# Kernel optimization log

Measured on AMD Instinct MI355X. Metric: run time of the kernel, lower is better.

Reference implementation:

```python
import jax, jax.numpy as jnp
import numpy as np

T = 4096          # time steps
I = 3             # input_size
R = 4096          # reservoir_size
LEAK = 0.1        # leaking_rate
RHO = 0.9         # spectral_radius
SPARSITY = 0.5


def setup_inputs() -> dict:
    key = jax.random.key(0)
    k1, k2, k3, k4 = jax.random.split(key, 4)
    x = jax.random.normal(k1, (T, I), dtype=jnp.float32)
    Win = jax.random.uniform(k2, (R, I), minval=-0.5, maxval=0.5, dtype=jnp.float32)
    Wh = jax.random.uniform(k3, (R, R), minval=-0.5, maxval=0.5, dtype=jnp.float32)
    mask = (jax.random.uniform(k4, (R, R)) < SPARSITY).astype(jnp.float32)
    Wh_np = np.asarray(Wh * mask, dtype=np.float64)
    # rescale to spectral radius RHO (power iteration estimate of dominant |eig|)
    v = np.random.default_rng(0).normal(size=R)
    rho = 1.0
    for _ in range(100):
        v = Wh_np @ v
        rho = np.linalg.norm(v)
        v = v / rho
    Wh = jnp.asarray(Wh_np * (RHO / rho), dtype=jnp.float32)
    return {"x": x, "Win": Win, "Wh": Wh}


def reference(x, Win, Wh):
    # Precompute all input projections in one GEMM: [T, R]
    ux = x @ Win.T

    def step(h, u):
        h_new = jnp.tanh(u + Wh @ h)
        h = LEAK * h + (1.0 - LEAK) * h_new
        return h, h

    h0 = jnp.zeros((Wh.shape[0],), dtype=x.dtype)
    _, hs = jax.lax.scan(step, h0, ux)   # hs: [T, R]
    return jnp.concatenate([hs, x], axis=1)  # H: [T, R + I]
```

## Files before the change

### kernel.cpp

```cpp
#include <hip/hip_runtime.h>
#include <cmath>


#define T_STEPS  4096
#define R_SIZE   4096
#define I_SIZE   3
#define OUT_COLS (R_SIZE + I_SIZE)
#define NB       256
#define BT       256
#define RPB      16
#define RPW      4
#define NREP     16
#define LEAK     0.1f

typedef _Float16 h2 __attribute__((ext_vector_type(2)));
typedef _Float16 h8 __attribute__((ext_vector_type(8)));
typedef unsigned u32x2 __attribute__((ext_vector_type(2)));
typedef unsigned u32x4 __attribute__((ext_vector_type(4)));

__device__ __forceinline__ float fdot2f(h2 a, h2 b, float c) {
#if __has_builtin(__builtin_amdgcn_fdot2)
    return __builtin_amdgcn_fdot2(a, b, c, false);
#else
    return c + (float)a[0] * (float)b[0] + (float)a[1] * (float)b[1];
#endif
}

__device__ __forceinline__ float fast_tanhf(float s) {
    float av = __builtin_fabsf(s);
    float e  = __builtin_amdgcn_exp2f(-2.8853900817779268f * av);
    float r  = (1.0f - e) * __builtin_amdgcn_rcpf(1.0f + e);
    return __builtin_copysignf(r, s);
}

__device__ __forceinline__ void poll16(const unsigned* p0, const unsigned* p1,
                                       const unsigned* p2, const unsigned* p3,
                                       u32x4& a0, u32x4& a1, u32x4& a2, u32x4& a3) {
    asm volatile(
        "global_load_dwordx4 %0, %4, off sc0 sc1\n\t"
        "global_load_dwordx4 %1, %5, off sc0 sc1\n\t"
        "global_load_dwordx4 %2, %6, off sc0 sc1\n\t"
        "global_load_dwordx4 %3, %7, off sc0 sc1\n\t"
        "s_waitcnt vmcnt(0)"
        : "=&v"(a0), "=&v"(a1), "=&v"(a2), "=&v"(a3)
        : "v"(p0), "v"(p1), "v"(p2), "v"(p3)
        : "memory");
}

__device__ __forceinline__ unsigned tagbad4(const u32x4& a, unsigned tg2) {
    unsigned t01 = __builtin_amdgcn_perm(a[1], a[0], 0x07060302u) ^ tg2;
    unsigned t23 = __builtin_amdgcn_perm(a[3], a[2], 0x07060302u) ^ tg2;
    return t01 | t23;
}
__device__ __forceinline__ int check16(const u32x4& a0, const u32x4& a1,
                                       const u32x4& a2, const u32x4& a3,
                                       unsigned tg2) {
    unsigned bad = tagbad4(a0, tg2) | tagbad4(a1, tg2) |
                   tagbad4(a2, tg2) | tagbad4(a3, tg2);
    return bad == 0u;
}

template<int CTRL>
__device__ __forceinline__ float dpp_ror_add(float a) {
    int r = __builtin_amdgcn_update_dpp(0, __builtin_bit_cast(int, a),
                                        CTRL, 0xF, 0xF, false);
    return a + __builtin_bit_cast(float, r);
}
__device__ __forceinline__ float wave_sum(float a, int idx32, int idx48) {
    a = dpp_ror_add<0x128>(a);
    a = dpp_ror_add<0x124>(a);
    a = dpp_ror_add<0x122>(a);
    a = dpp_ror_add<0x121>(a);
    int ai = __builtin_bit_cast(int, a);
    float b = __builtin_bit_cast(float, __builtin_amdgcn_ds_swizzle(ai, 0x401F));
    float c = __builtin_bit_cast(float, __builtin_amdgcn_ds_bpermute(idx32, ai));
    float d = __builtin_bit_cast(float, __builtin_amdgcn_ds_bpermute(idx48, ai));
    return (a + b) + (c + d);
}

__global__ void __launch_bounds__(BT, 1) esn_kernel(
    const float* __restrict__ Wh,
    const float* __restrict__ Win,
    const float* __restrict__ x,
    float* __restrict__ out,
    unsigned* __restrict__ ex0,
    unsigned* __restrict__ ex1,
    unsigned rep_mask)
{
    __shared__ alignas(16) unsigned short hl[R_SIZE];
    __shared__ float xs[T_STEPS * I_SIZE];

    const int tid  = threadIdx.x;
    const int bid  = blockIdx.x;
    const int wv   = tid >> 6;
    const int lane = tid & 63;
    const int r0   = bid * RPB;
    const int idx32 = ((lane ^ 32) << 2);
    const int idx48 = ((lane ^ 48) << 2);

    h8 wreg[RPW * 8];
    #pragma unroll
    for (int rr = 0; rr < RPW; ++rr) {
        const float* src = Wh + (size_t)(r0 + wv * RPW + rr) * R_SIZE;
        #pragma unroll
        for (int j = 0; j < 8; ++j) {
            int e = (j * 64 + lane) * 8;
            float4 a = *(const float4*)(src + e);
            float4 b = *(const float4*)(src + e + 4);
            h8 hv;
            hv[0] = (_Float16)a.x; hv[1] = (_Float16)a.y;
            hv[2] = (_Float16)a.z; hv[3] = (_Float16)a.w;
            hv[4] = (_Float16)b.x; hv[5] = (_Float16)b.y;
            hv[6] = (_Float16)b.z; hv[7] = (_Float16)b.w;
            wreg[rr * 8 + j] = hv;
        }
    }

    for (int i = tid; i < T_STEPS * I_SIZE; i += BT) xs[i] = x[i];

    float win0 = 0.f, win1 = 0.f, win2 = 0.f;
    if (lane < RPW) {
        int r = r0 + wv * RPW + lane;
        win0 = Win[(size_t)r * I_SIZE + 0];
        win1 = Win[(size_t)r * I_SIZE + 1];
        win2 = Win[(size_t)r * I_SIZE + 2];
    }
    float hown = 0.0f;

    const unsigned rep  = (unsigned)bid & rep_mask;
    const unsigned nrep = rep_mask + 1u;
    const unsigned* pa[2][4];
    #pragma unroll
    for (int m = 0; m < 4; ++m) {
        pa[0][m] = ex0 + rep * R_SIZE + m * 1024 + tid * 4;
        pa[1][m] = ex1 + rep * R_SIZE + m * 1024 + tid * 4;
    }

    __syncthreads();

    unsigned long long tgt = 0;
    unsigned P = 0;

    for (int t = 0; t < T_STEPS; ++t) {
        const int par = t & 1;
        unsigned* __restrict__ exw = par ? ex0 : ex1;

        float u = 0.0f;
        if (lane < RPW)
            u = xs[t * 3 + 0] * win0 + xs[t * 3 + 1] * win1 +
                xs[t * 3 + 2] * win2;

        if (P) {
            for (int i = 0; i < 4096; ++i) {
                if (__builtin_amdgcn_s_memrealtime() >= tgt) break;
                __builtin_amdgcn_s_sleep(2);
            }
        }

        u32x4 a0, a1, a2, a3;
        const unsigned tg2 = (unsigned)t * 0x00010001u;
        poll16(pa[par][0], pa[par][1], pa[par][2], pa[par][3], a0, a1, a2, a3);
        int ok = check16(a0, a1, a2, a3, tg2);
        const int missed = !__all(ok);
        if (missed) {
            do {
                __builtin_amdgcn_s_sleep(1);
                if (!ok) {
                    poll16(pa[par][0], pa[par][1], pa[par][2], pa[par][3],
                           a0, a1, a2, a3);
                    ok = check16(a0, a1, a2, a3, tg2);
                }
            } while (!__all(ok));
        }

        {
            u32x4 aa[4] = {a0, a1, a2, a3};
            #pragma unroll
            for (int m = 0; m < 4; ++m) {
                u32x2 w;
                w[0] = __builtin_amdgcn_perm(aa[m][1], aa[m][0], 0x05040100u);
                w[1] = __builtin_amdgcn_perm(aa[m][3], aa[m][2], 0x05040100u);
                *(u32x2*)&hl[m * 1024 + tid * 4] = w;
            }
        }
        __syncthreads();

        h8 hreg[8];
        const h8* hl8 = (const h8*)hl;
        #pragma unroll
        for (int j = 0; j < 8; ++j) hreg[j] = hl8[j * 64 + lane];

        float acc[RPW];
        #pragma unroll
        for (int rr = 0; rr < RPW; ++rr) {
            float a = 0.0f;
            #pragma unroll
            for (int j = 0; j < 8; ++j) {
                h8 w8 = wreg[rr * 8 + j];
                h8 hh = hreg[j];
                a = fdot2f(__builtin_shufflevector(w8, w8, 0, 1),
                           __builtin_shufflevector(hh, hh, 0, 1), a);
                a = fdot2f(__builtin_shufflevector(w8, w8, 2, 3),
                           __builtin_shufflevector(hh, hh, 2, 3), a);
                a = fdot2f(__builtin_shufflevector(w8, w8, 4, 5),
                           __builtin_shufflevector(hh, hh, 4, 5), a);
                a = fdot2f(__builtin_shufflevector(w8, w8, 6, 7),
                           __builtin_shufflevector(hh, hh, 6, 7), a);
            }
            acc[rr] = wave_sum(a, idx32, idx48);
        }

        float hv = 0.0f;
        unsigned word = 0;
        if (lane < RPW) {
            float a = (lane == 0) ? acc[0]
                    : (lane == 1) ? acc[1]
                    : (lane == 2) ? acc[2] : acc[3];
            float hn = fast_tanhf(u + a);
            hv = LEAK * hown + (1.0f - LEAK) * hn;
            hown = hv;
            word = ((unsigned)(t + 1) << 16) |
                   (unsigned)__builtin_bit_cast(unsigned short, (_Float16)hv);
        }
        unsigned w0 = __shfl(word, 0, 64);
        unsigned w1 = __shfl(word, 1, 64);
        unsigned w2 = __shfl(word, 2, 64);
        unsigned w3 = __shfl(word, 3, 64);
        if ((unsigned)lane < nrep) {
            u32x4 pw = {w0, w1, w2, w3};
            unsigned* dst = exw + (unsigned)lane * R_SIZE + r0 + wv * RPW;
            asm volatile("global_store_dwordx4 %0, %1, off sc0 sc1"
                         :: "v"(dst), "v"(pw) : "memory");
        }

        {
            unsigned long long nowp = __builtin_amdgcn_s_memrealtime();
            P = missed ? (P + 8u > 2048u ? 2048u : P + 8u)
                       : (P >= 2u ? P - 2u : 0u);
            tgt = nowp + P;
        }

        if (lane < RPW) {
            out[(size_t)t * OUT_COLS + (r0 + wv * RPW + lane)] = hv;
        }
    }
}

__global__ void copy_x_kernel(const float* __restrict__ x, float* __restrict__ out) {
    int i = blockIdx.x * blockDim.x + threadIdx.x;
    if (i < T_STEPS * I_SIZE) {
        int t = i / I_SIZE, c = i % I_SIZE;
        out[(size_t)t * OUT_COLS + R_SIZE + c] = x[i];
    }
}

extern "C" void kernel_launch(void* const* d_in, const int* in_sizes, int n_in,
                              void* d_out, int out_size, void* d_ws, size_t ws_size,
                              hipStream_t stream) {
    const float* x   = (const float*)d_in[0];
    const float* Win = (const float*)d_in[1];
    const float* Wh  = (const float*)d_in[2];
    float* out = (float*)d_out;

    size_t need16 = (size_t)2 * 16 * R_SIZE * sizeof(unsigned);
    size_t need8  = (size_t)2 *  8 * R_SIZE * sizeof(unsigned);
    unsigned nrep = (ws_size >= need16) ? 16u : (ws_size >= need8 ? 8u : 1u);
    unsigned rep_mask = nrep - 1u;
    unsigned* ex0 = (unsigned*)d_ws;
    unsigned* ex1 = ex0 + (size_t)nrep * R_SIZE;

    (void)hipMemsetAsync(d_ws, 0, (size_t)2 * nrep * R_SIZE * sizeof(unsigned),
                         stream);

    copy_x_kernel<<<dim3((T_STEPS * I_SIZE + BT - 1) / BT), dim3(BT), 0, stream>>>(x, out);

    void* args[] = {(void*)&Wh, (void*)&Win, (void*)&x, (void*)&out,
                    (void*)&ex0, (void*)&ex1, (void*)&rep_mask};
    hipError_t e = hipLaunchCooperativeKernel((void*)esn_kernel, dim3(NB), dim3(BT),
                                              args, 0, stream);
    if (e != hipSuccess) {
        esn_kernel<<<dim3(NB), dim3(BT), 0, stream>>>(Wh, Win, x, out,
                                                      ex0, ex1, rep_mask);
    }
}
```

Baseline: 8.116 ms.

## Split dot-product across K within block, drop LDS staging of hidden state

Each thread now keeps 16 rows by 16 contiguous columns of Wh in registers and dots them directly with the polled hidden-state values. This removes the LDS staging of the full state vector and the barrier that followed it. Partial sums are reduced within 16-lane groups by DPP, then combined across the block through a small double-buffered LDS array after one barrier. Wave 0 alone computes tanh, publishes the tagged words and writes the output. The step's critical path now runs through that cross-wave reduction and a single-wave publish.

```diff
diff --git a/kernel.cpp b/kernel.cpp
--- a/kernel.cpp
+++ b/kernel.cpp
@@ -9,13 +9,10 @@
 #define NB       256
 #define BT       256
 #define RPB      16
-#define RPW      4
 #define NREP     16
 #define LEAK     0.1f
 
 typedef _Float16 h2 __attribute__((ext_vector_type(2)));
-typedef _Float16 h8 __attribute__((ext_vector_type(8)));
-typedef unsigned u32x2 __attribute__((ext_vector_type(2)));
 typedef unsigned u32x4 __attribute__((ext_vector_type(4)));
 
 __device__ __forceinline__ float fdot2f(h2 a, h2 b, float c) {
@@ -66,16 +63,16 @@
                                         CTRL, 0xF, 0xF, false);
     return a + __builtin_bit_cast(float, r);
 }
-__device__ __forceinline__ float wave_sum(float a, int idx32, int idx48) {
+__device__ __forceinline__ float group16_sum(float a) {
     a = dpp_ror_add<0x128>(a);
     a = dpp_ror_add<0x124>(a);
     a = dpp_ror_add<0x122>(a);
     a = dpp_ror_add<0x121>(a);
-    int ai = __builtin_bit_cast(int, a);
-    float b = __builtin_bit_cast(float, __builtin_amdgcn_ds_swizzle(ai, 0x401F));
-    float c = __builtin_bit_cast(float, __builtin_amdgcn_ds_bpermute(idx32, ai));
-    float d = __builtin_bit_cast(float, __builtin_amdgcn_ds_bpermute(idx48, ai));
-    return (a + b) + (c + d);
+    return a;
+}
+
+__device__ __forceinline__ h2 lo_pair(unsigned wa, unsigned wb) {
+    return __builtin_bit_cast(h2, __builtin_amdgcn_perm(wb, wa, 0x05040100u));
 }
 
 __global__ void __launch_bounds__(BT, 1) esn_kernel(
@@ -87,7 +84,7 @@
     unsigned* __restrict__ ex1,
     unsigned rep_mask)
 {
-    __shared__ alignas(16) unsigned short hl[R_SIZE];
+    __shared__ float comb[2][16][16];
     __shared__ float xs[T_STEPS * I_SIZE];
 
     const int tid  = threadIdx.x;
@@ -95,46 +92,40 @@
     const int wv   = tid >> 6;
     const int lane = tid & 63;
     const int r0   = bid * RPB;
-    const int idx32 = ((lane ^ 32) << 2);
-    const int idx48 = ((lane ^ 48) << 2);
-
-    h8 wreg[RPW * 8];
+
+    h2 wreg[RPB][8];
     #pragma unroll
-    for (int rr = 0; rr < RPW; ++rr) {
-        const float* src = Wh + (size_t)(r0 + wv * RPW + rr) * R_SIZE;
-        #pragma unroll
-        for (int j = 0; j < 8; ++j) {
-            int e = (j * 64 + lane) * 8;
-            float4 a = *(const float4*)(src + e);
-            float4 b = *(const float4*)(src + e + 4);
-            h8 hv;
-            hv[0] = (_Float16)a.x; hv[1] = (_Float16)a.y;
-            hv[2] = (_Float16)a.z; hv[3] = (_Float16)a.w;
-            hv[4] = (_Float16)b.x; hv[5] = (_Float16)b.y;
-            hv[6] = (_Float16)b.z; hv[7] = (_Float16)b.w;
-            wreg[rr * 8 + j] = hv;
-        }
+    for (int r = 0; r < RPB; ++r) {
+        const float* src = Wh + (size_t)(r0 + r) * R_SIZE + wv * 1024 + lane * 16;
+        float4 A = *(const float4*)(src + 0);
+        float4 B = *(const float4*)(src + 4);
+        float4 C = *(const float4*)(src + 8);
+        float4 D = *(const float4*)(src + 12);
+        wreg[r][0][0] = (_Float16)A.x; wreg[r][0][1] = (_Float16)A.y;
+        wreg[r][1][0] = (_Float16)A.z; wreg[r][1][1] = (_Float16)A.w;
+        wreg[r][2][0] = (_Float16)B.x; wreg[r][2][1] = (_Float16)B.y;
+        wreg[r][3][0] = (_Float16)B.z; wreg[r][3][1] = (_Float16)B.w;
+        wreg[r][4][0] = (_Float16)C.x; wreg[r][4][1] = (_Float16)C.y;
+        wreg[r][5][0] = (_Float16)C.z; wreg[r][5][1] = (_Float16)C.w;
+        wreg[r][6][0] = (_Float16)D.x; wreg[r][6][1] = (_Float16)D.y;
+        wreg[r][7][0] = (_Float16)D.z; wreg[r][7][1] = (_Float16)D.w;
     }
 
     for (int i = tid; i < T_STEPS * I_SIZE; i += BT) xs[i] = x[i];
 
     float win0 = 0.f, win1 = 0.f, win2 = 0.f;
-    if (lane < RPW) {
-        int r = r0 + wv * RPW + lane;
+    if (wv == 0 && lane < RPB) {
+        int r = r0 + lane;
         win0 = Win[(size_t)r * I_SIZE + 0];
         win1 = Win[(size_t)r * I_SIZE + 1];
         win2 = Win[(size_t)r * I_SIZE + 2];
     }
     float hown = 0.0f;
 
-    const unsigned rep  = (unsigned)bid & rep_mask;
-    const unsigned nrep = rep_mask + 1u;
-    const unsigned* pa[2][4];
-    #pragma unroll
-    for (int m = 0; m < 4; ++m) {
-        pa[0][m] = ex0 + rep * R_SIZE + m * 1024 + tid * 4;
-        pa[1][m] = ex1 + rep * R_SIZE + m * 1024 + tid * 4;
-    }
+    const unsigned rep = (unsigned)bid & rep_mask;
+    const unsigned* pb[2];
+    pb[0] = ex0 + rep * R_SIZE + wv * 1024 + lane * 16;
+    pb[1] = ex1 + rep * R_SIZE + wv * 1024 + lane * 16;
 
     __syncthreads();
 
@@ -146,7 +137,7 @@
         unsigned* __restrict__ exw = par ? ex0 : ex1;
 
         float u = 0.0f;
-        if (lane < RPW)
+        if (wv == 0 && lane < RPB)
             u = xs[t * 3 + 0] * win0 + xs[t * 3 + 1] * win1 +
                 xs[t * 3 + 2] * win2;
 
@@ -159,78 +150,71 @@
 
         u32x4 a0, a1, a2, a3;
         const unsigned tg2 = (unsigned)t * 0x00010001u;
-        poll16(pa[par][0], pa[par][1], pa[par][2], pa[par][3], a0, a1, a2, a3);
+        const unsigned* pp = pb[par];
+        poll16(pp, pp + 4, pp + 8, pp + 12, a0, a1, a2, a3);
         int ok = check16(a0, a1, a2, a3, tg2);
         const int missed = !__all(ok);
         if (missed) {
             do {
                 __builtin_amdgcn_s_sleep(1);
                 if (!ok) {
-                    poll16(pa[par][0], pa[par][1], pa[par][2], pa[par][3],
-                           a0, a1, a2, a3);
+                    poll16(pp, pp + 4, pp + 8, pp + 12, a0, a1, a2, a3);
                     ok = check16(a0, a1, a2, a3, tg2);
                 }
             } while (!__all(ok));
         }
 
-        {
-            u32x4 aa[4] = {a0, a1, a2, a3};
+        h2 hh[8];
+        hh[0] = lo_pair(a0[0], a0[1]); hh[1] = lo_pair(a0[2], a0[3]);
+        hh[2] = lo_pair(a1[0], a1[1]); hh[3] = lo_pair(a1[2], a1[3]);
+        hh[4] = lo_pair(a2[0], a2[1]); hh[5] = lo_pair(a2[2], a2[3]);
+        hh[6] = lo_pair(a3[0], a3[1]); hh[7] = lo_pair(a3[2], a3[3]);
+
+        float acc[RPB];
+        #pragma unroll
+        for (int r = 0; r < RPB; ++r) {
+            float s = 0.0f;
             #pragma unroll
-            for (int m = 0; m < 4; ++m) {
-                u32x2 w;
-                w[0] = __builtin_amdgcn_perm(aa[m][1], aa[m][0], 0x05040100u);
-                w[1] = __builtin_amdgcn_perm(aa[m][3], aa[m][2], 0x05040100u);
-                *(u32x2*)&hl[m * 1024 + tid * 4] = w;
+            for (int j = 0; j < 8; ++j)
+                s = fdot2f(wreg[r][j], hh[j], s);
+            acc[r] = group16_sum(s);
+        }
+
+        if ((lane & 15) == 0) {
+            const int c = wv * 4 + (lane >> 4);
+            float4* q = (float4*)&comb[par][c][0];
+            q[0] = make_float4(acc[0],  acc[1],  acc[2],  acc[3]);
+            q[1] = make_float4(acc[4],  acc[5],  acc[6],  acc[7]);
+            q[2] = make_float4(acc[8],  acc[9],  acc[10], acc[11]);
+            q[3] = make_float4(acc[12], acc[13], acc[14], acc[15]);
+        }
+        __syncthreads();
+
+        if (wv == 0) {
+            float hv = 0.0f;
+            unsigned word = 0;
+            if (lane < RPB) {
+                float s = 0.0f;
+                #pragma unroll
+                for (int c = 0; c < 16; ++c) s += comb[par][c][lane];
+                float hn = fast_tanhf(u + s);
+                hv = LEAK * hown + (1.0f - LEAK) * hn;
+                hown = hv;
+                word = ((unsigned)(t + 1) << 16) |
+                       (unsigned)__builtin_bit_cast(unsigned short, (_Float16)hv);
             }
-        }
-        __syncthreads();
-
-        h8 hreg[8];
-        const h8* hl8 = (const h8*)hl;
-        #pragma unroll
-        for (int j = 0; j < 8; ++j) hreg[j] = hl8[j * 64 + lane];
-
-        float acc[RPW];
-        #pragma unroll
-        for (int rr = 0; rr < RPW; ++rr) {
-            float a = 0.0f;
-            #pragma unroll
-            for (int j = 0; j < 8; ++j) {
-                h8 w8 = wreg[rr * 8 + j];
-                h8 hh = hreg[j];
-                a = fdot2f(__builtin_shufflevector(w8, w8, 0, 1),
-                           __builtin_shufflevector(hh, hh, 0, 1), a);
-                a = fdot2f(__builtin_shufflevector(w8, w8, 2, 3),
-                           __builtin_shufflevector(hh, hh, 2, 3), a);
-                a = fdot2f(__builtin_shufflevector(w8, w8, 4, 5),
-                           __builtin_shufflevector(hh, hh, 4, 5), a);
-                a = fdot2f(__builtin_shufflevector(w8, w8, 6, 7),
-                           __builtin_shufflevector(hh, hh, 6, 7), a);
+            const int rq = (lane & 3) * 4;
+            unsigned w0 = __shfl(word, rq + 0, 64);
+            unsigned w1 = __shfl(word, rq + 1, 64);
+            unsigned w2 = __shfl(word, rq + 2, 64);
+            unsigned w3 = __shfl(word, rq + 3, 64);
+            if ((unsigned)(lane >> 2) <= rep_mask) {
+                u32x4 pw = {w0, w1, w2, w3};
+                unsigned* dst = exw + (unsigned)(lane >> 2) * R_SIZE + r0 + rq;
+                asm volatile("global_store_dwordx4 %0, %1, off sc0 sc1"
+                             :: "v"(dst), "v"(pw) : "memory");
             }
-            acc[rr] = wave_sum(a, idx32, idx48);
-        }
-
-        float hv = 0.0f;
-        unsigned word = 0;
-        if (lane < RPW) {
-            float a = (lane == 0) ? acc[0]
-                    : (lane == 1) ? acc[1]
-                    : (lane == 2) ? acc[2] : acc[3];
-            float hn = fast_tanhf(u + a);
-            hv = LEAK * hown + (1.0f - LEAK) * hn;
-            hown = hv;
-            word = ((unsigned)(t + 1) << 16) |
-                   (unsigned)__builtin_bit_cast(unsigned short, (_Float16)hv);
-        }
-        unsigned w0 = __shfl(word, 0, 64);
-        unsigned w1 = __shfl(word, 1, 64);
-        unsigned w2 = __shfl(word, 2, 64);
-        unsigned w3 = __shfl(word, 3, 64);
-        if ((unsigned)lane < nrep) {
-            u32x4 pw = {w0, w1, w2, w3};
-            unsigned* dst = exw + (unsigned)lane * R_SIZE + r0 + wv * RPW;
-            asm volatile("global_store_dwordx4 %0, %1, off sc0 sc1"
-                         :: "v"(dst), "v"(pw) : "memory");
+            if (lane < RPB) out[(size_t)t * OUT_COLS + (r0 + lane)] = hv;
         }
 
         {
@@ -238,10 +222,6 @@
             P = missed ? (P + 8u > 2048u ? 2048u : P + 8u)
                        : (P >= 2u ? P - 2u : 0u);
             tgt = nowp + P;
-        }
-
-        if (lane < RPW) {
-            out[(size_t)t * OUT_COLS + (r0 + wv * RPW + lane)] = hv;
         }
     }
 }
```

Result: slower. 9.321 ms (+14.8%).
